# Performance work log

Measured on AMD Instinct MI355X. Metric: run time of the kernel, lower is better.

Reference implementation:

```python
import jax, jax.numpy as jnp
import numpy as np

EPS = 1e-8


def setup_inputs() -> dict:
    key = jax.random.key(0)
    ks = jax.random.split(key, 8)
    B, N, D = 8, 1024, 256
    x = jax.random.normal(ks[0], (B, N, D), dtype=jnp.float32)
    y = jax.random.normal(ks[1], (B, N, D), dtype=jnp.float32)
    coords = jax.random.normal(ks[2], (N, N, 6), dtype=jnp.float32)
    # xavier-ish init for U, kaiming-ish for S1/S2
    U = jax.random.normal(ks[3], (D, D), dtype=jnp.float32) * (1.0 / np.sqrt(D))
    S1 = jax.random.normal(ks[4], (D, 1), dtype=jnp.float32)
    S2 = jax.random.normal(ks[5], (D, 1), dtype=jnp.float32)
    gating = jnp.asarray(1.0, dtype=jnp.float32)
    h_temp = jnp.asarray(0.1, dtype=jnp.float32)
    p_temp = jnp.asarray(1.0, dtype=jnp.float32)
    # trunc_normal_(a=0, b=1): std-normal truncated to [0, 1]
    pos_emb = jax.random.truncated_normal(ks[6], 0.0, 1.0, (N, 6, 1)).astype(jnp.float32)
    return {"x": x, "y": y, "coords": coords, "U": U, "S1": S1, "S2": S2,
            "gating": gating, "h_temp": h_temp, "p_temp": p_temp, "pos_emb": pos_emb}


def _spectral(x, U, S):
    # x @ U.T @ diag(|S|) @ U  ==  ((x @ U.T) * |S|) @ U
    s = jnp.abs(S[:, 0])
    return ((x @ U.T) * s) @ U


def reference(x, y, coords, U, S1, S2, gating, h_temp, p_temp, pos_emb):
    B, N, D = x.shape
    scale = D ** (-0.5)
    xs = jnp.stack([_spectral(x, U, S1), _spectral(x, U, S2)], axis=1)  # [B,2,N,D]
    # patch attention scores: [B,2,N,N]
    patch_score = jax.nn.softmax(jnp.einsum('bknd,bmd->bknm', xs, y) * scale, axis=-1)
    # positional scores, shared across batch and the 2 spectral branches: [N,N]
    pos_logits = -jnp.abs(p_temp) * jnp.einsum('nmc,ncq->nm', coords, pos_emb)
    pos_score = jax.nn.softmax(pos_logits, axis=-1)
    g = jax.nn.sigmoid(gating)
    attn = (1.0 - g) * patch_score + g * pos_score[None, None]  # [B,2,N,N]
    # entropy over key axis -> [B,N,2]
    entropy = jnp.sum(-attn * jnp.log(attn + EPS), axis=-1).transpose(0, 2, 1)
    hmap = 2.0 - 2.0 * jax.nn.sigmoid(h_temp * entropy)  # [B,N,2]
    fgbg = hmap[..., 0] >= hmap[..., 1]
    route = jax.lax.stop_gradient(
        jnp.stack([fgbg, ~fgbg], axis=-1).astype(hmap.dtype))  # [B,N,2]
    heat_map = jnp.sum(hmap * route, axis=-1, keepdims=True)  # [B,N,1]
    attn_sel = jnp.sum(attn * route.transpose(0, 2, 1)[..., None], axis=1)  # [B,N,N]
    out = attn_sel @ y  # [B,N,D]
    return (out, heat_map)
```

## Files before the change

### kernel.cpp

```cpp
#include <hip/hip_runtime.h>
#include <hip/hip_bf16.h>
#include <stdint.h>


#define NB 8
#define NN_ 1024
#define ND 256

typedef __bf16 bf16x8 __attribute__((ext_vector_type(8)));
typedef __bf16 bf16x4 __attribute__((ext_vector_type(4)));
typedef float f32x4 __attribute__((ext_vector_type(4)));

__device__ inline void gl_lds(const __bf16* g, __bf16* l) {
    auto gp = (const __attribute__((address_space(1))) uint32_t*)(uintptr_t)g;
    auto lp = (__attribute__((address_space(3))) uint32_t*)(uintptr_t)l;
    __builtin_amdgcn_global_load_lds(gp, lp, 16, 0, 0);
}

__device__ inline float wred_sum(float v) {
#pragma unroll
    for (int o = 32; o; o >>= 1) v += __shfl_xor(v, o, 64);
    return v;
}
__device__ inline float wred_max(float v) {
#pragma unroll
    for (int o = 32; o; o >>= 1) v = fmaxf(v, __shfl_xor(v, o, 64));
    return v;
}
__device__ inline float bred_sum(float v, float* red) {
    v = wred_sum(v);
    int w = threadIdx.x >> 6;
    __syncthreads();
    if ((threadIdx.x & 63) == 0) red[w] = v;
    __syncthreads();
    return red[0] + red[1] + red[2] + red[3];
}
__device__ inline float bred_max(float v, float* red) {
    v = wred_max(v);
    int w = threadIdx.x >> 6;
    __syncthreads();
    if ((threadIdx.x & 63) == 0) red[w] = v;
    __syncthreads();
    return fmaxf(fmaxf(red[0], red[1]), fmaxf(red[2], red[3]));
}

__global__ __launch_bounds__(256) void pos_kernel(
    const float* __restrict__ coords, const float* __restrict__ pos_emb,
    const float* __restrict__ p_temp, float* __restrict__ posS) {
    __shared__ float red[4];
    const int n = blockIdx.x;
    const int tid = threadIdx.x;
    const float pt = -fabsf(p_temp[0]);
    float pe[6];
#pragma unroll
    for (int c = 0; c < 6; ++c) pe[c] = pos_emb[n * 6 + c];
    const float* cr = coords + (long)n * NN_ * 6;
    float l[4];
#pragma unroll
    for (int j = 0; j < 4; ++j) {
        const int m = j * 256 + tid;
        const float2* cp = (const float2*)(cr + (long)m * 6);
        float2 c0 = cp[0], c1 = cp[1], c2 = cp[2];
        l[j] = pt * (c0.x * pe[0] + c0.y * pe[1] + c1.x * pe[2] +
                     c1.y * pe[3] + c2.x * pe[4] + c2.y * pe[5]);
    }
    float mx = fmaxf(fmaxf(l[0], l[1]), fmaxf(l[2], l[3]));
    mx = bred_max(mx, red);
    float e[4], s = 0.f;
#pragma unroll
    for (int j = 0; j < 4; ++j) { e[j] = expf(l[j] - mx); s += e[j]; }
    s = bred_sum(s, red);
    const float inv = 1.f / s;
#pragma unroll
    for (int j = 0; j < 4; ++j) posS[(long)n * NN_ + j * 256 + tid] = e[j] * inv;
}

__global__ __launch_bounds__(256) void conv_split(
    const float* __restrict__ src, __bf16* __restrict__ hi,
    __bf16* __restrict__ lo, int n4) {
    int i = blockIdx.x * 256 + threadIdx.x;
    const int stride = gridDim.x * 256;
    for (; i < n4; i += stride) {
        float4 v = ((const float4*)src)[i];
        bf16x4 h, l;
        h[0] = (__bf16)v.x; l[0] = (__bf16)(v.x - (float)h[0]);
        h[1] = (__bf16)v.y; l[1] = (__bf16)(v.y - (float)h[1]);
        h[2] = (__bf16)v.z; l[2] = (__bf16)(v.z - (float)h[2]);
        h[3] = (__bf16)v.w; l[3] = (__bf16)(v.w - (float)h[3]);
        ((bf16x4*)hi)[i] = h;
        ((bf16x4*)lo)[i] = l;
    }
}

__global__ __launch_bounds__(256) void build_M(
    const float* __restrict__ U, const float* __restrict__ S1,
    const float* __restrict__ S2, __bf16* __restrict__ Mh,
    __bf16* __restrict__ Ml) {
    const int n = blockIdx.x, j = threadIdx.x;
    float a1 = 0.f, a2 = 0.f;
    for (int c = 0; c < ND; ++c) {
        const float un = U[c * ND + n];
        const float uj = U[c * ND + j];
        a1 = fmaf(fabsf(S1[c]) * un, uj, a1);
        a2 = fmaf(fabsf(S2[c]) * un, uj, a2);
    }
    const __bf16 h1 = (__bf16)a1, h2 = (__bf16)a2;
    Mh[n * ND + j] = h1;            Ml[n * ND + j] = (__bf16)(a1 - (float)h1);
    Mh[65536 + n * ND + j] = h2;    Ml[65536 + n * ND + j] = (__bf16)(a2 - (float)h2);
}

__global__ __launch_bounds__(256) void prep_y(
    const float* __restrict__ y, __bf16* __restrict__ yt,
    __bf16* __restrict__ Yh, __bf16* __restrict__ Yl) {
    __shared__ __bf16 t[64][72];
    const int b = blockIdx.z;
    const int m0 = blockIdx.x * 64, d0 = blockIdx.y * 64;
    const int tid = threadIdx.x;
    const int c = tid & 15;
    const int r = tid >> 4;
#pragma unroll
    for (int p = 0; p < 4; ++p) {
        const int row = r + p * 16;
        const long gi = ((long)b * NN_ + m0 + row) * ND + d0 + c * 4;
        float4 v = *(const float4*)(y + gi);
        bf16x4 h, l;
        h[0] = (__bf16)v.x; l[0] = (__bf16)(v.x - (float)h[0]);
        h[1] = (__bf16)v.y; l[1] = (__bf16)(v.y - (float)h[1]);
        h[2] = (__bf16)v.z; l[2] = (__bf16)(v.z - (float)h[2]);
        h[3] = (__bf16)v.w; l[3] = (__bf16)(v.w - (float)h[3]);
        *(bf16x4*)(Yh + gi) = h;
        *(bf16x4*)(Yl + gi) = l;
        t[c * 4 + 0][row] = h[0]; t[c * 4 + 1][row] = h[1];
        t[c * 4 + 2][row] = h[2]; t[c * 4 + 3][row] = h[3];
    }
    __syncthreads();
#pragma unroll
    for (int p = 0; p < 4; ++p) {
        const int d = r + p * 16;
        bf16x4 o;
        o[0] = t[d][c * 4 + 0]; o[1] = t[d][c * 4 + 1];
        o[2] = t[d][c * 4 + 2]; o[3] = t[d][c * 4 + 3];
        *(bf16x4*)(yt + ((long)b * ND + d0 + d) * NN_ + m0 + c * 4) = o;
    }
}

template <int BN, bool SPLIT, int OUTM>
__global__ __launch_bounds__(256) void mgemm(
    const __bf16* __restrict__ Ah, const __bf16* __restrict__ Al,
    const __bf16* __restrict__ Bh, const __bf16* __restrict__ Bl,
    float* __restrict__ C, __bf16* __restrict__ Ch, __bf16* __restrict__ Cl,
    int M, int N, int K,
    long sA1, long sA2, int divA, long sB1, int divB, long sC, float alpha) {
    constexpr int BM = 128, BK = 32;
    constexpr int NBUF = SPLIT ? 2 : 1;
    constexpr int NF = BN / 32;
    __shared__ __bf16 As[NBUF * BM * BK];
    __shared__ __bf16 Bs[NBUF * BN * BK];

    const int z = blockIdx.z;
    const long aoff = (long)(z / divA) * sA1 + (long)(z % divA) * sA2;
    const long boff = (long)(z / divB) * sB1;
    Ah += aoff; if (SPLIT) Al += aoff;
    Bh += boff; if (SPLIT) Bl += boff;

    const int tid = threadIdx.x;
    const int bm = blockIdx.y * BM, bn = blockIdx.x * BN;
    const int wave = tid >> 6, lane = tid & 63;
    const int wm = wave >> 1, wn = wave & 1;
    const int quad = lane >> 4, l16 = lane & 15;

    f32x4 acc[4][NF];
#pragma unroll
    for (int i = 0; i < 4; ++i)
#pragma unroll
        for (int j = 0; j < NF; ++j) acc[i][j] = (f32x4){0.f, 0.f, 0.f, 0.f};

    const int srow = lane >> 2;
    const int slot = lane & 3;

    for (int k0 = 0; k0 < K; k0 += BK) {
        __syncthreads();
#pragma unroll
        for (int i = 0; i < 2; ++i) {
            const int r0 = wave * 32 + i * 16;
            const int row = r0 + srow;
            const int chunk = slot ^ ((row >> 1) & 3);
            const long g = (long)(bm + row) * K + k0 + chunk * 8;
            gl_lds(Ah + g, &As[r0 * 32]);
            if (SPLIT) gl_lds(Al + g, &As[BM * BK + r0 * 32]);
        }
        if (BN == 128) {
#pragma unroll
            for (int i = 0; i < 2; ++i) {
                const int r0 = wave * 32 + i * 16;
                const int row = r0 + srow;
                const int chunk = slot ^ ((row >> 1) & 3);
                const long g = (long)(bn + row) * K + k0 + chunk * 8;
                gl_lds(Bh + g, &Bs[r0 * 32]);
                if (SPLIT) gl_lds(Bl + g, &Bs[BN * BK + r0 * 32]);
            }
        } else {
            const int r0 = wave * 16;
            const int row = r0 + srow;
            const int chunk = slot ^ ((row >> 1) & 3);
            const long g = (long)(bn + row) * K + k0 + chunk * 8;
            gl_lds(Bh + g, &Bs[r0 * 32]);
            if (SPLIT) gl_lds(Bl + g, &Bs[BN * BK + r0 * 32]);
        }
        __syncthreads();

        bf16x8 a_h[4], a_l[4], b_h[NF], b_l[NF];
#pragma unroll
        for (int mi = 0; mi < 4; ++mi) {
            const int row = wm * 64 + mi * 16 + l16;
            const int off = row * 32 + ((quad ^ ((row >> 1) & 3)) * 8);
            a_h[mi] = *(const bf16x8*)&As[off];
            if (SPLIT) a_l[mi] = *(const bf16x8*)&As[BM * BK + off];
        }
#pragma unroll
        for (int ni = 0; ni < NF; ++ni) {
            const int row = wn * (BN / 2) + ni * 16 + l16;
            const int off = row * 32 + ((quad ^ ((row >> 1) & 3)) * 8);
            b_h[ni] = *(const bf16x8*)&Bs[off];
            if (SPLIT) b_l[ni] = *(const bf16x8*)&Bs[BN * BK + off];
        }
#pragma unroll
        for (int mi = 0; mi < 4; ++mi)
#pragma unroll
            for (int ni = 0; ni < NF; ++ni) {
                acc[mi][ni] = __builtin_amdgcn_mfma_f32_16x16x32_bf16(
                    a_h[mi], b_h[ni], acc[mi][ni], 0, 0, 0);
                if (SPLIT) {
                    acc[mi][ni] = __builtin_amdgcn_mfma_f32_16x16x32_bf16(
                        a_h[mi], b_l[ni], acc[mi][ni], 0, 0, 0);
                    acc[mi][ni] = __builtin_amdgcn_mfma_f32_16x16x32_bf16(
                        a_l[mi], b_h[ni], acc[mi][ni], 0, 0, 0);
                }
            }
    }

    C += (long)z * sC; Ch += (long)z * sC; Cl += (long)z * sC;
#pragma unroll
    for (int mi = 0; mi < 4; ++mi) {
        const int row0 = bm + wm * 64 + mi * 16 + quad * 4;
#pragma unroll
        for (int ni = 0; ni < NF; ++ni) {
            const int col = bn + wn * (BN / 2) + ni * 16 + l16;
#pragma unroll
            for (int r = 0; r < 4; ++r) {
                const float v = acc[mi][ni][r] * alpha;
                const long idx = (long)(row0 + r) * N + col;
                if (OUTM == 0) {
                    C[idx] = v;
                } else {
                    const __bf16 h = (__bf16)v;
                    Ch[idx] = h;
                    Cl[idx] = (__bf16)(v - (float)h);
                }
            }
        }
    }
}

__global__ __launch_bounds__(256, 1) void mega_kernel(
    const __bf16* __restrict__ XSh, const __bf16* __restrict__ XSl,
    const __bf16* __restrict__ Yh, const __bf16* __restrict__ Yl,
    const __bf16* __restrict__ yt, const float* __restrict__ pos,
    const float* __restrict__ gating, const float* __restrict__ h_temp,
    float* __restrict__ heat, float* __restrict__ out) {
    extern __shared__ char smem[];
    __bf16* Pl  = (__bf16*)smem;
    float* red0 = (float*)(smem + 66048);
    float* red1 = red0 + 256;
    float* red2 = red1 + 256;

    const int b  = blockIdx.x & 7;
    const int n0 = (blockIdx.x >> 3) * 32;
    const int tid = threadIdx.x;
    const int wave = tid >> 6, lane = tid & 63;
    const int quad = lane >> 4, l16 = lane & 15;
    const int wcol = wave * 256;

    const __bf16* Ahp = XSh + ((long)b * NN_ + n0) * ND;
    const __bf16* Alp = XSl + ((long)b * NN_ + n0) * ND;
    const __bf16* Bhp = Yh + ((long)b * NN_ + wcol) * ND;
    const __bf16* Blp = Yl + ((long)b * NN_ + wcol) * ND;

    f32x4 acc[2][2][16];
#pragma unroll
    for (int br = 0; br < 2; ++br)
#pragma unroll
        for (int mi = 0; mi < 2; ++mi)
#pragma unroll
            for (int ni = 0; ni < 16; ++ni)
                acc[br][mi][ni] = (f32x4){0.f, 0.f, 0.f, 0.f};

    for (int k0 = 0; k0 < ND; k0 += 32) {
        bf16x8 ah[2][2], al[2][2];
#pragma unroll
        for (int br = 0; br < 2; ++br)
#pragma unroll
            for (int mi = 0; mi < 2; ++mi) {
                const long o = (long)br * (NB * NN_ * ND) +
                               (long)(mi * 16 + l16) * ND + k0 + quad * 8;
                ah[br][mi] = *(const bf16x8*)(Ahp + o);
                al[br][mi] = *(const bf16x8*)(Alp + o);
            }
#pragma unroll
        for (int ni = 0; ni < 16; ++ni) {
            const long o = (long)(ni * 16 + l16) * ND + k0 + quad * 8;
            bf16x8 bh = *(const bf16x8*)(Bhp + o);
            bf16x8 bl = *(const bf16x8*)(Blp + o);
#pragma unroll
            for (int br = 0; br < 2; ++br)
#pragma unroll
                for (int mi = 0; mi < 2; ++mi) {
                    acc[br][mi][ni] = __builtin_amdgcn_mfma_f32_16x16x32_bf16(
                        ah[br][mi], bh, acc[br][mi][ni], 0, 0, 0);
                    acc[br][mi][ni] = __builtin_amdgcn_mfma_f32_16x16x32_bf16(
                        ah[br][mi], bl, acc[br][mi][ni], 0, 0, 0);
                    acc[br][mi][ni] = __builtin_amdgcn_mfma_f32_16x16x32_bf16(
                        al[br][mi], bh, acc[br][mi][ni], 0, 0, 0);
                }
        }
    }

#pragma unroll
    for (int br = 0; br < 2; ++br)
#pragma unroll
        for (int mi = 0; mi < 2; ++mi)
#pragma unroll
            for (int ni = 0; ni < 16; ++ni)
#pragma unroll
                for (int rr = 0; rr < 4; ++rr)
                    acc[br][mi][ni][rr] *= 0.0625f;

    float mx[2][2][4];
#pragma unroll
    for (int br = 0; br < 2; ++br)
#pragma unroll
        for (int mi = 0; mi < 2; ++mi)
#pragma unroll
            for (int rr = 0; rr < 4; ++rr) {
                float m = -3.4e38f;
#pragma unroll
                for (int ni = 0; ni < 16; ++ni) m = fmaxf(m, acc[br][mi][ni][rr]);
                mx[br][mi][rr] = m;
            }
#pragma unroll
    for (int o = 1; o < 16; o <<= 1)
#pragma unroll
        for (int br = 0; br < 2; ++br)
#pragma unroll
            for (int mi = 0; mi < 2; ++mi)
#pragma unroll
                for (int rr = 0; rr < 4; ++rr)
                    mx[br][mi][rr] = fmaxf(mx[br][mi][rr],
                                           __shfl_xor(mx[br][mi][rr], o, 64));
    if (l16 == 0)
#pragma unroll
        for (int br = 0; br < 2; ++br)
#pragma unroll
            for (int mi = 0; mi < 2; ++mi)
#pragma unroll
                for (int rr = 0; rr < 4; ++rr)
                    red0[(wave * 2 + br) * 32 + mi * 16 + quad * 4 + rr] = mx[br][mi][rr];
    __syncthreads();
#pragma unroll
    for (int br = 0; br < 2; ++br)
#pragma unroll
        for (int mi = 0; mi < 2; ++mi)
#pragma unroll
            for (int rr = 0; rr < 4; ++rr) {
                const int ri = mi * 16 + quad * 4 + rr;
                float m = red0[(0 * 2 + br) * 32 + ri];
                m = fmaxf(m, red0[(1 * 2 + br) * 32 + ri]);
                m = fmaxf(m, red0[(2 * 2 + br) * 32 + ri]);
                m = fmaxf(m, red0[(3 * 2 + br) * 32 + ri]);
                mx[br][mi][rr] = m;
            }

    float sm[2][2][4];
#pragma unroll
    for (int br = 0; br < 2; ++br)
#pragma unroll
        for (int mi = 0; mi < 2; ++mi)
#pragma unroll
            for (int rr = 0; rr < 4; ++rr) {
                float s = 0.f;
#pragma unroll
                for (int ni = 0; ni < 16; ++ni) {
                    const float e = __expf(acc[br][mi][ni][rr] - mx[br][mi][rr]);
                    acc[br][mi][ni][rr] = e;
                    s += e;
                }
                sm[br][mi][rr] = s;
            }
#pragma unroll
    for (int o = 1; o < 16; o <<= 1)
#pragma unroll
        for (int br = 0; br < 2; ++br)
#pragma unroll
            for (int mi = 0; mi < 2; ++mi)
#pragma unroll
                for (int rr = 0; rr < 4; ++rr)
                    sm[br][mi][rr] += __shfl_xor(sm[br][mi][rr], o, 64);
    if (l16 == 0)
#pragma unroll
        for (int br = 0; br < 2; ++br)
#pragma unroll
            for (int mi = 0; mi < 2; ++mi)
#pragma unroll
                for (int rr = 0; rr < 4; ++rr)
                    red1[(wave * 2 + br) * 32 + mi * 16 + quad * 4 + rr] = sm[br][mi][rr];
    __syncthreads();
    float inv[2][2][4];
#pragma unroll
    for (int br = 0; br < 2; ++br)
#pragma unroll
        for (int mi = 0; mi < 2; ++mi)
#pragma unroll
            for (int rr = 0; rr < 4; ++rr) {
                const int ri = mi * 16 + quad * 4 + rr;
                const float s = red1[(0 * 2 + br) * 32 + ri] + red1[(1 * 2 + br) * 32 + ri] +
                                red1[(2 * 2 + br) * 32 + ri] + red1[(3 * 2 + br) * 32 + ri];
                inv[br][mi][rr] = 1.f / s;
            }

    const float g = 1.f / (1.f + __expf(-gating[0]));
    const float cg = 1.f - g;
    float ent[2][2][4];
#pragma unroll
    for (int br = 0; br < 2; ++br)
#pragma unroll
        for (int mi = 0; mi < 2; ++mi)
#pragma unroll
            for (int rr = 0; rr < 4; ++rr) ent[br][mi][rr] = 0.f;
#pragma unroll
    for (int mi = 0; mi < 2; ++mi)
#pragma unroll
        for (int ni = 0; ni < 16; ++ni)
#pragma unroll
            for (int rr = 0; rr < 4; ++rr) {
                const int ri = mi * 16 + quad * 4 + rr;
                const float pv = pos[(long)(n0 + ri) * NN_ + wcol + ni * 16 + l16];
#pragma unroll
                for (int br = 0; br < 2; ++br) {
                    const float a = cg * acc[br][mi][ni][rr] * inv[br][mi][rr] + g * pv;
                    acc[br][mi][ni][rr] = a;
                    ent[br][mi][rr] -= a * __logf(a + 1e-8f);
                }
            }
#pragma unroll
    for (int o = 1; o < 16; o <<= 1)
#pragma unroll
        for (int br = 0; br < 2; ++br)
#pragma unroll
            for (int mi = 0; mi < 2; ++mi)
#pragma unroll
                for (int rr = 0; rr < 4; ++rr)
                    ent[br][mi][rr] += __shfl_xor(ent[br][mi][rr], o, 64);
    if (l16 == 0)
#pragma unroll
        for (int br = 0; br < 2; ++br)
#pragma unroll
            for (int mi = 0; mi < 2; ++mi)
#pragma unroll
                for (int rr = 0; rr < 4; ++rr)
                    red2[(wave * 2 + br) * 32 + mi * 16 + quad * 4 + rr] = ent[br][mi][rr];
    __syncthreads();

    const float ht = h_temp[0];
    float fsel[2][4];
#pragma unroll
    for (int mi = 0; mi < 2; ++mi)
#pragma unroll
        for (int rr = 0; rr < 4; ++rr) {
            const int ri = mi * 16 + quad * 4 + rr;
            const float e0 = red2[0 * 32 + ri] + red2[2 * 32 + ri] +
                             red2[4 * 32 + ri] + red2[6 * 32 + ri];
            const float e1 = red2[1 * 32 + ri] + red2[3 * 32 + ri] +
                             red2[5 * 32 + ri] + red2[7 * 32 + ri];
            const float hm0 = 2.f - 2.f / (1.f + __expf(-ht * e0));
            const float hm1 = 2.f - 2.f / (1.f + __expf(-ht * e1));
            const bool fg = (hm0 >= hm1);
            fsel[mi][rr] = fg ? 1.f : 0.f;
            if (wave == 0 && l16 == 0)
                heat[(long)b * NN_ + n0 + ri] = fg ? hm0 : hm1;
        }
#pragma unroll
    for (int mi = 0; mi < 2; ++mi)
#pragma unroll
        for (int ni = 0; ni < 16; ++ni)
#pragma unroll
            for (int rr = 0; rr < 4; ++rr) {
                const int ri = mi * 16 + quad * 4 + rr;
                const float v = fsel[mi][rr] != 0.f ? acc[0][mi][ni][rr]
                                                    : acc[1][mi][ni][rr];
                Pl[ri * 1032 + wcol + ni * 16 + l16] = (__bf16)v;
            }
    __syncthreads();

    f32x4 oacc[2][4];
#pragma unroll
    for (int mi = 0; mi < 2; ++mi)
#pragma unroll
        for (int nd = 0; nd < 4; ++nd) oacc[mi][nd] = (f32x4){0.f, 0.f, 0.f, 0.f};
    const __bf16* Bo = yt + ((long)b * ND + wave * 64) * NN_;
    for (int k0 = 0; k0 < NN_; k0 += 32) {
        bf16x8 pa[2];
#pragma unroll
        for (int mi = 0; mi < 2; ++mi)
            pa[mi] = *(const bf16x8*)&Pl[(mi * 16 + l16) * 1032 + k0 + quad * 8];
#pragma unroll
        for (int nd = 0; nd < 4; ++nd) {
            bf16x8 bo = *(const bf16x8*)(Bo + (long)(nd * 16 + l16) * NN_ + k0 + quad * 8);
#pragma unroll
            for (int mi = 0; mi < 2; ++mi)
                oacc[mi][nd] = __builtin_amdgcn_mfma_f32_16x16x32_bf16(
                    pa[mi], bo, oacc[mi][nd], 0, 0, 0);
        }
    }
#pragma unroll
    for (int mi = 0; mi < 2; ++mi)
#pragma unroll
        for (int nd = 0; nd < 4; ++nd)
#pragma unroll
            for (int r = 0; r < 4; ++r)
                out[((long)b * NN_ + n0 + mi * 16 + quad * 4 + r) * ND +
                    wave * 64 + nd * 16 + l16] = oacc[mi][nd][r];
}

extern "C" void kernel_launch(void* const* d_in, const int* in_sizes, int n_in,
                              void* d_out, int out_size, void* d_ws, size_t ws_size,
                              hipStream_t stream) {
    const float* x      = (const float*)d_in[0];
    const float* y      = (const float*)d_in[1];
    const float* coords = (const float*)d_in[2];
    const float* U      = (const float*)d_in[3];
    const float* S1p    = (const float*)d_in[4];
    const float* S2p    = (const float*)d_in[5];
    const float* gating = (const float*)d_in[6];
    const float* h_temp = (const float*)d_in[7];
    const float* p_temp = (const float*)d_in[8];
    const float* pos_emb= (const float*)d_in[9];

    float* out  = (float*)d_out;
    float* heat = out + (long)NB * NN_ * ND;

    char* ws = (char*)d_ws;
    const long MB = 1 << 20;
    float*  pos = (float*)(ws);
    __bf16* Xh  = (__bf16*)(ws + 4 * MB);
    __bf16* Xl  = (__bf16*)(ws + 8 * MB);
    __bf16* XSh = (__bf16*)(ws + 12 * MB);
    __bf16* XSl = (__bf16*)(ws + 20 * MB);
    __bf16* yt  = (__bf16*)(ws + 28 * MB);
    __bf16* Yh  = (__bf16*)(ws + 32 * MB);
    __bf16* Yl  = (__bf16*)(ws + 36 * MB);
    __bf16* Mh  = (__bf16*)(ws + 40 * MB);
    __bf16* Ml  = Mh + 2 * 65536;

    const long ND2 = (long)NN_ * ND;
    const long BND = (long)NB * ND2;

    pos_kernel<<<dim3(NN_), 256, 0, stream>>>(coords, pos_emb, p_temp, pos);
    conv_split<<<dim3(2048), 256, 0, stream>>>(x, Xh, Xl, (int)(BND / 4));
    prep_y<<<dim3(16, 4, NB), 256, 0, stream>>>(y, yt, Yh, Yl);
    build_M<<<dim3(ND), ND, 0, stream>>>(U, S1p, S2p, Mh, Ml);

    mgemm<64, true, 1><<<dim3(4, 64, 2), 256, 0, stream>>>(
        Xh, Xl, Mh, Ml, nullptr, XSh, XSl, NB * NN_, ND, ND,
        0, 0, 1, 65536, 1, BND, 1.0f);

    hipFuncSetAttribute((const void*)mega_kernel,
                        hipFuncAttributeMaxDynamicSharedMemorySize, 69632);
    mega_kernel<<<dim3(256), 256, 69632, stream>>>(
        XSh, XSl, Yh, Yl, yt, pos, gating, h_temp, heat, out);

    (void)in_sizes; (void)n_in; (void)out_size; (void)ws_size;
}
```

Before: 229.6 us.

## Fuse prep kernels into one launch and halve mega_kernel row tile

Merges the four preprocessing kernels (pos softmax, x split, y split/transpose, M build) into a single launch that dispatches on block index, removing three kernel launches and their serialization gaps. The main fused attention kernel now processes 16 query rows per block instead of 32, doubling the grid to 512 blocks. It also switches to static shared memory and allows two blocks per CU, to improve occupancy and CU coverage. The trade-off is that each block re-reads the full Y tiles for only half as many rows, doubling B-operand traffic per output row.

```diff
diff --git a/kernel.cpp b/kernel.cpp
--- a/kernel.cpp
+++ b/kernel.cpp
@@ -27,120 +27,110 @@
     for (int o = 32; o; o >>= 1) v = fmaxf(v, __shfl_xor(v, o, 64));
     return v;
 }
-__device__ inline float bred_sum(float v, float* red) {
-    v = wred_sum(v);
-    int w = threadIdx.x >> 6;
-    __syncthreads();
-    if ((threadIdx.x & 63) == 0) red[w] = v;
-    __syncthreads();
-    return red[0] + red[1] + red[2] + red[3];
-}
-__device__ inline float bred_max(float v, float* red) {
-    v = wred_max(v);
-    int w = threadIdx.x >> 6;
-    __syncthreads();
-    if ((threadIdx.x & 63) == 0) red[w] = v;
-    __syncthreads();
-    return fmaxf(fmaxf(red[0], red[1]), fmaxf(red[2], red[3]));
-}
-
-__global__ __launch_bounds__(256) void pos_kernel(
+
+__global__ __launch_bounds__(256) void prep_kernel(
     const float* __restrict__ coords, const float* __restrict__ pos_emb,
-    const float* __restrict__ p_temp, float* __restrict__ posS) {
-    __shared__ float red[4];
-    const int n = blockIdx.x;
+    const float* __restrict__ p_temp, const float* __restrict__ x,
+    const float* __restrict__ y, const float* __restrict__ U,
+    const float* __restrict__ S1, const float* __restrict__ S2,
+    float* __restrict__ posS, __bf16* __restrict__ Xh, __bf16* __restrict__ Xl,
+    __bf16* __restrict__ yt, __bf16* __restrict__ Yh, __bf16* __restrict__ Yl,
+    __bf16* __restrict__ Mh, __bf16* __restrict__ Ml) {
+    __shared__ char sm[9216 + 64];
+    const int bid = blockIdx.x;
     const int tid = threadIdx.x;
-    const float pt = -fabsf(p_temp[0]);
-    float pe[6];
-#pragma unroll
-    for (int c = 0; c < 6; ++c) pe[c] = pos_emb[n * 6 + c];
-    const float* cr = coords + (long)n * NN_ * 6;
-    float l[4];
-#pragma unroll
-    for (int j = 0; j < 4; ++j) {
-        const int m = j * 256 + tid;
-        const float2* cp = (const float2*)(cr + (long)m * 6);
-        float2 c0 = cp[0], c1 = cp[1], c2 = cp[2];
-        l[j] = pt * (c0.x * pe[0] + c0.y * pe[1] + c1.x * pe[2] +
-                     c1.y * pe[3] + c2.x * pe[4] + c2.y * pe[5]);
-    }
-    float mx = fmaxf(fmaxf(l[0], l[1]), fmaxf(l[2], l[3]));
-    mx = bred_max(mx, red);
-    float e[4], s = 0.f;
-#pragma unroll
-    for (int j = 0; j < 4; ++j) { e[j] = expf(l[j] - mx); s += e[j]; }
-    s = bred_sum(s, red);
-    const float inv = 1.f / s;
-#pragma unroll
-    for (int j = 0; j < 4; ++j) posS[(long)n * NN_ + j * 256 + tid] = e[j] * inv;
-}
-
-__global__ __launch_bounds__(256) void conv_split(
-    const float* __restrict__ src, __bf16* __restrict__ hi,
-    __bf16* __restrict__ lo, int n4) {
-    int i = blockIdx.x * 256 + threadIdx.x;
-    const int stride = gridDim.x * 256;
-    for (; i < n4; i += stride) {
-        float4 v = ((const float4*)src)[i];
-        bf16x4 h, l;
-        h[0] = (__bf16)v.x; l[0] = (__bf16)(v.x - (float)h[0]);
-        h[1] = (__bf16)v.y; l[1] = (__bf16)(v.y - (float)h[1]);
-        h[2] = (__bf16)v.z; l[2] = (__bf16)(v.z - (float)h[2]);
-        h[3] = (__bf16)v.w; l[3] = (__bf16)(v.w - (float)h[3]);
-        ((bf16x4*)hi)[i] = h;
-        ((bf16x4*)lo)[i] = l;
-    }
-}
-
-__global__ __launch_bounds__(256) void build_M(
-    const float* __restrict__ U, const float* __restrict__ S1,
-    const float* __restrict__ S2, __bf16* __restrict__ Mh,
-    __bf16* __restrict__ Ml) {
-    const int n = blockIdx.x, j = threadIdx.x;
-    float a1 = 0.f, a2 = 0.f;
-    for (int c = 0; c < ND; ++c) {
-        const float un = U[c * ND + n];
-        const float uj = U[c * ND + j];
-        a1 = fmaf(fabsf(S1[c]) * un, uj, a1);
-        a2 = fmaf(fabsf(S2[c]) * un, uj, a2);
-    }
-    const __bf16 h1 = (__bf16)a1, h2 = (__bf16)a2;
-    Mh[n * ND + j] = h1;            Ml[n * ND + j] = (__bf16)(a1 - (float)h1);
-    Mh[65536 + n * ND + j] = h2;    Ml[65536 + n * ND + j] = (__bf16)(a2 - (float)h2);
-}
-
-__global__ __launch_bounds__(256) void prep_y(
-    const float* __restrict__ y, __bf16* __restrict__ yt,
-    __bf16* __restrict__ Yh, __bf16* __restrict__ Yl) {
-    __shared__ __bf16 t[64][72];
-    const int b = blockIdx.z;
-    const int m0 = blockIdx.x * 64, d0 = blockIdx.y * 64;
-    const int tid = threadIdx.x;
-    const int c = tid & 15;
-    const int r = tid >> 4;
-#pragma unroll
-    for (int p = 0; p < 4; ++p) {
-        const int row = r + p * 16;
-        const long gi = ((long)b * NN_ + m0 + row) * ND + d0 + c * 4;
-        float4 v = *(const float4*)(y + gi);
-        bf16x4 h, l;
-        h[0] = (__bf16)v.x; l[0] = (__bf16)(v.x - (float)h[0]);
-        h[1] = (__bf16)v.y; l[1] = (__bf16)(v.y - (float)h[1]);
-        h[2] = (__bf16)v.z; l[2] = (__bf16)(v.z - (float)h[2]);
-        h[3] = (__bf16)v.w; l[3] = (__bf16)(v.w - (float)h[3]);
-        *(bf16x4*)(Yh + gi) = h;
-        *(bf16x4*)(Yl + gi) = l;
-        t[c * 4 + 0][row] = h[0]; t[c * 4 + 1][row] = h[1];
-        t[c * 4 + 2][row] = h[2]; t[c * 4 + 3][row] = h[3];
-    }
-    __syncthreads();
-#pragma unroll
-    for (int p = 0; p < 4; ++p) {
-        const int d = r + p * 16;
-        bf16x4 o;
-        o[0] = t[d][c * 4 + 0]; o[1] = t[d][c * 4 + 1];
-        o[2] = t[d][c * 4 + 2]; o[3] = t[d][c * 4 + 3];
-        *(bf16x4*)(yt + ((long)b * ND + d0 + d) * NN_ + m0 + c * 4) = o;
+
+    if (bid < 1024) {
+        float* red = (float*)sm;
+        const int n = bid;
+        const float pt = -fabsf(p_temp[0]);
+        float pe[6];
+#pragma unroll
+        for (int c = 0; c < 6; ++c) pe[c] = pos_emb[n * 6 + c];
+        const float* cr = coords + (long)n * NN_ * 6;
+        float l[4];
+#pragma unroll
+        for (int j = 0; j < 4; ++j) {
+            const int m = j * 256 + tid;
+            const float2* cp = (const float2*)(cr + (long)m * 6);
+            float2 c0 = cp[0], c1 = cp[1], c2 = cp[2];
+            l[j] = pt * (c0.x * pe[0] + c0.y * pe[1] + c1.x * pe[2] +
+                         c1.y * pe[3] + c2.x * pe[4] + c2.y * pe[5]);
+        }
+        float mx = fmaxf(fmaxf(l[0], l[1]), fmaxf(l[2], l[3]));
+        mx = wred_max(mx);
+        __syncthreads();
+        if ((tid & 63) == 0) red[tid >> 6] = mx;
+        __syncthreads();
+        mx = fmaxf(fmaxf(red[0], red[1]), fmaxf(red[2], red[3]));
+        float e[4], s = 0.f;
+#pragma unroll
+        for (int j = 0; j < 4; ++j) { e[j] = __expf(l[j] - mx); s += e[j]; }
+        s = wred_sum(s);
+        __syncthreads();
+        if ((tid & 63) == 0) red[4 + (tid >> 6)] = s;
+        __syncthreads();
+        s = red[4] + red[5] + red[6] + red[7];
+        const float inv = 1.f / s;
+#pragma unroll
+        for (int j = 0; j < 4; ++j)
+            posS[(long)n * NN_ + j * 256 + tid] = e[j] * inv;
+    } else if (bid < 1536) {
+        const int n4 = NB * NN_ * ND / 4;
+        int i = (bid - 1024) * 256 + tid;
+        for (; i < n4; i += 512 * 256) {
+            float4 v = ((const float4*)x)[i];
+            bf16x4 h, l;
+            h[0] = (__bf16)v.x; l[0] = (__bf16)(v.x - (float)h[0]);
+            h[1] = (__bf16)v.y; l[1] = (__bf16)(v.y - (float)h[1]);
+            h[2] = (__bf16)v.z; l[2] = (__bf16)(v.z - (float)h[2]);
+            h[3] = (__bf16)v.w; l[3] = (__bf16)(v.w - (float)h[3]);
+            ((bf16x4*)Xh)[i] = h;
+            ((bf16x4*)Xl)[i] = l;
+        }
+    } else if (bid < 2048) {
+        __bf16 (*t)[72] = (__bf16(*)[72])sm;
+        const int rem = bid - 1536;
+        const int b = rem >> 6;
+        const int m0 = (rem & 15) * 64, d0 = ((rem >> 4) & 3) * 64;
+        const int c = tid & 15;
+        const int r = tid >> 4;
+#pragma unroll
+        for (int p = 0; p < 4; ++p) {
+            const int row = r + p * 16;
+            const long gi = ((long)b * NN_ + m0 + row) * ND + d0 + c * 4;
+            float4 v = *(const float4*)(y + gi);
+            bf16x4 h, l;
+            h[0] = (__bf16)v.x; l[0] = (__bf16)(v.x - (float)h[0]);
+            h[1] = (__bf16)v.y; l[1] = (__bf16)(v.y - (float)h[1]);
+            h[2] = (__bf16)v.z; l[2] = (__bf16)(v.z - (float)h[2]);
+            h[3] = (__bf16)v.w; l[3] = (__bf16)(v.w - (float)h[3]);
+            *(bf16x4*)(Yh + gi) = h;
+            *(bf16x4*)(Yl + gi) = l;
+            t[c * 4 + 0][row] = h[0]; t[c * 4 + 1][row] = h[1];
+            t[c * 4 + 2][row] = h[2]; t[c * 4 + 3][row] = h[3];
+        }
+        __syncthreads();
+#pragma unroll
+        for (int p = 0; p < 4; ++p) {
+            const int d = r + p * 16;
+            bf16x4 o;
+            o[0] = t[d][c * 4 + 0]; o[1] = t[d][c * 4 + 1];
+            o[2] = t[d][c * 4 + 2]; o[3] = t[d][c * 4 + 3];
+            *(bf16x4*)(yt + ((long)b * ND + d0 + d) * NN_ + m0 + c * 4) = o;
+        }
+    } else {
+        const int n = bid - 2048, j = tid;
+        float a1 = 0.f, a2 = 0.f;
+        for (int c = 0; c < ND; ++c) {
+            const float un = U[c * ND + n];
+            const float uj = U[c * ND + j];
+            a1 = fmaf(fabsf(S1[c]) * un, uj, a1);
+            a2 = fmaf(fabsf(S2[c]) * un, uj, a2);
+        }
+        const __bf16 h1 = (__bf16)a1, h2 = (__bf16)a2;
+        Mh[n * ND + j] = h1;           Ml[n * ND + j] = (__bf16)(a1 - (float)h1);
+        Mh[65536 + n * ND + j] = h2;   Ml[65536 + n * ND + j] = (__bf16)(a2 - (float)h2);
     }
 }
 
@@ -262,273 +252,214 @@
     }
 }
 
-__global__ __launch_bounds__(256, 1) void mega_kernel(
+__global__ __launch_bounds__(256, 2) void mega_kernel(
     const __bf16* __restrict__ XSh, const __bf16* __restrict__ XSl,
     const __bf16* __restrict__ Yh, const __bf16* __restrict__ Yl,
     const __bf16* __restrict__ yt, const float* __restrict__ pos,
     const float* __restrict__ gating, const float* __restrict__ h_temp,
     float* __restrict__ heat, float* __restrict__ out) {
-    extern __shared__ char smem[];
-    __bf16* Pl  = (__bf16*)smem;
-    float* red0 = (float*)(smem + 66048);
-    float* red1 = red0 + 256;
-    float* red2 = red1 + 256;
+    __shared__ __bf16 Pl[16 * 1032];
+    __shared__ float red0[128], red1[128], red2[128];
 
     const int b  = blockIdx.x & 7;
-    const int n0 = (blockIdx.x >> 3) * 32;
+    const int n0 = (blockIdx.x >> 3) * 16;
     const int tid = threadIdx.x;
     const int wave = tid >> 6, lane = tid & 63;
     const int quad = lane >> 4, l16 = lane & 15;
     const int wcol = wave * 256;
+    const long BNDe = (long)NB * NN_ * ND;
 
     const __bf16* Ahp = XSh + ((long)b * NN_ + n0) * ND;
     const __bf16* Alp = XSl + ((long)b * NN_ + n0) * ND;
     const __bf16* Bhp = Yh + ((long)b * NN_ + wcol) * ND;
     const __bf16* Blp = Yl + ((long)b * NN_ + wcol) * ND;
 
-    f32x4 acc[2][2][16];
+    f32x4 acc[2][16];
 #pragma unroll
     for (int br = 0; br < 2; ++br)
 #pragma unroll
-        for (int mi = 0; mi < 2; ++mi)
-#pragma unroll
-            for (int ni = 0; ni < 16; ++ni)
-                acc[br][mi][ni] = (f32x4){0.f, 0.f, 0.f, 0.f};
+        for (int ni = 0; ni < 16; ++ni) acc[br][ni] = (f32x4){0.f, 0.f, 0.f, 0.f};
 
     for (int k0 = 0; k0 < ND; k0 += 32) {
-        bf16x8 ah[2][2], al[2][2];
-#pragma unroll
-        for (int br = 0; br < 2; ++br)
-#pragma unroll
-            for (int mi = 0; mi < 2; ++mi) {
-                const long o = (long)br * (NB * NN_ * ND) +
-                               (long)(mi * 16 + l16) * ND + k0 + quad * 8;
-                ah[br][mi] = *(const bf16x8*)(Ahp + o);
-                al[br][mi] = *(const bf16x8*)(Alp + o);
-            }
+        bf16x8 ah[2], al[2];
+#pragma unroll
+        for (int br = 0; br < 2; ++br) {
+            const long o = (long)br * BNDe + (long)l16 * ND + k0 + quad * 8;
+            ah[br] = *(const bf16x8*)(Ahp + o);
+            al[br] = *(const bf16x8*)(Alp + o);
+        }
 #pragma unroll
         for (int ni = 0; ni < 16; ++ni) {
             const long o = (long)(ni * 16 + l16) * ND + k0 + quad * 8;
             bf16x8 bh = *(const bf16x8*)(Bhp + o);
             bf16x8 bl = *(const bf16x8*)(Blp + o);
 #pragma unroll
-            for (int br = 0; br < 2; ++br)
-#pragma unroll
-                for (int mi = 0; mi < 2; ++mi) {
-                    acc[br][mi][ni] = __builtin_amdgcn_mfma_f32_16x16x32_bf16(
-                        ah[br][mi], bh, acc[br][mi][ni], 0, 0, 0);
-                    acc[br][mi][ni] = __builtin_amdgcn_mfma_f32_16x16x32_bf16(
-                        ah[br][mi], bl, acc[br][mi][ni], 0, 0, 0);
-                    acc[br][mi][ni] = __builtin_amdgcn_mfma_f32_16x16x32_bf16(
-                        al[br][mi], bh, acc[br][mi][ni], 0, 0, 0);
-                }
+            for (int br = 0; br < 2; ++br) {
+                acc[br][ni] = __builtin_amdgcn_mfma_f32_16x16x32_bf16(
+                    ah[br], bh, acc[br][ni], 0, 0, 0);
+                acc[br][ni] = __builtin_amdgcn_mfma_f32_16x16x32_bf16(
+                    ah[br], bl, acc[br][ni], 0, 0, 0);
+                acc[br][ni] = __builtin_amdgcn_mfma_f32_16x16x32_bf16(
+                    al[br], bh, acc[br][ni], 0, 0, 0);
+            }
         }
     }
 
+    float mx[2][4];
 #pragma unroll
     for (int br = 0; br < 2; ++br)
 #pragma unroll
-        for (int mi = 0; mi < 2; ++mi)
-#pragma unroll
-            for (int ni = 0; ni < 16; ++ni)
-#pragma unroll
-                for (int rr = 0; rr < 4; ++rr)
-                    acc[br][mi][ni][rr] *= 0.0625f;
-
-    float mx[2][2][4];
+        for (int rr = 0; rr < 4; ++rr) {
+            float m = -3.4e38f;
+#pragma unroll
+            for (int ni = 0; ni < 16; ++ni) {
+                acc[br][ni][rr] *= 0.0625f;
+                m = fmaxf(m, acc[br][ni][rr]);
+            }
+            mx[br][rr] = m;
+        }
+#pragma unroll
+    for (int o = 1; o < 16; o <<= 1)
+#pragma unroll
+        for (int br = 0; br < 2; ++br)
+#pragma unroll
+            for (int rr = 0; rr < 4; ++rr)
+                mx[br][rr] = fmaxf(mx[br][rr], __shfl_xor(mx[br][rr], o, 64));
+    if (l16 == 0)
+#pragma unroll
+        for (int br = 0; br < 2; ++br)
+#pragma unroll
+            for (int rr = 0; rr < 4; ++rr)
+                red0[(wave * 2 + br) * 16 + quad * 4 + rr] = mx[br][rr];
+    __syncthreads();
 #pragma unroll
     for (int br = 0; br < 2; ++br)
 #pragma unroll
-        for (int mi = 0; mi < 2; ++mi)
-#pragma unroll
-            for (int rr = 0; rr < 4; ++rr) {
-                float m = -3.4e38f;
-#pragma unroll
-                for (int ni = 0; ni < 16; ++ni) m = fmaxf(m, acc[br][mi][ni][rr]);
-                mx[br][mi][rr] = m;
-            }
+        for (int rr = 0; rr < 4; ++rr) {
+            const int ri = quad * 4 + rr;
+            float m = red0[(0 + br) * 16 + ri];
+            m = fmaxf(m, red0[(2 + br) * 16 + ri]);
+            m = fmaxf(m, red0[(4 + br) * 16 + ri]);
+            m = fmaxf(m, red0[(6 + br) * 16 + ri]);
+            mx[br][rr] = m;
+        }
+
+    float sm[2][4];
+#pragma unroll
+    for (int br = 0; br < 2; ++br)
+#pragma unroll
+        for (int rr = 0; rr < 4; ++rr) {
+            float s = 0.f;
+#pragma unroll
+            for (int ni = 0; ni < 16; ++ni) {
+                const float e = __expf(acc[br][ni][rr] - mx[br][rr]);
+                acc[br][ni][rr] = e;
+                s += e;
+            }
+            sm[br][rr] = s;
+        }
 #pragma unroll
     for (int o = 1; o < 16; o <<= 1)
 #pragma unroll
         for (int br = 0; br < 2; ++br)
 #pragma unroll
-            for (int mi = 0; mi < 2; ++mi)
-#pragma unroll
-                for (int rr = 0; rr < 4; ++rr)
-                    mx[br][mi][rr] = fmaxf(mx[br][mi][rr],
-                                           __shfl_xor(mx[br][mi][rr], o, 64));
+            for (int rr = 0; rr < 4; ++rr)
+                sm[br][rr] += __shfl_xor(sm[br][rr], o, 64);
     if (l16 == 0)
 #pragma unroll
         for (int br = 0; br < 2; ++br)
 #pragma unroll
-            for (int mi = 0; mi < 2; ++mi)
-#pragma unroll
-                for (int rr = 0; rr < 4; ++rr)
-                    red0[(wave * 2 + br) * 32 + mi * 16 + quad * 4 + rr] = mx[br][mi][rr];
+            for (int rr = 0; rr < 4; ++rr)
+                red1[(wave * 2 + br) * 16 + quad * 4 + rr] = sm[br][rr];
     __syncthreads();
+    float inv[2][4];
 #pragma unroll
     for (int br = 0; br < 2; ++br)
 #pragma unroll
-        for (int mi = 0; mi < 2; ++mi)
-#pragma unroll
-            for (int rr = 0; rr < 4; ++rr) {
-                const int ri = mi * 16 + quad * 4 + rr;
-                float m = red0[(0 * 2 + br) * 32 + ri];
-                m = fmaxf(m, red0[(1 * 2 + br) * 32 + ri]);
-                m = fmaxf(m, red0[(2 * 2 + br) * 32 + ri]);
-                m = fmaxf(m, red0[(3 * 2 + br) * 32 + ri]);
-                mx[br][mi][rr] = m;
-            }
-
-    float sm[2][2][4];
-#pragma unroll
-    for (int br = 0; br < 2; ++br)
-#pragma unroll
-        for (int mi = 0; mi < 2; ++mi)
-#pragma unroll
-            for (int rr = 0; rr < 4; ++rr) {
-                float s = 0.f;
-#pragma unroll
-                for (int ni = 0; ni < 16; ++ni) {
-                    const float e = __expf(acc[br][mi][ni][rr] - mx[br][mi][rr]);
-                    acc[br][mi][ni][rr] = e;
-                    s += e;
-                }
-                sm[br][mi][rr] = s;
-            }
-#pragma unroll
-    for (int o = 1; o < 16; o <<= 1)
-#pragma unroll
-        for (int br = 0; br < 2; ++br)
-#pragma unroll
-            for (int mi = 0; mi < 2; ++mi)
-#pragma unroll
-                for (int rr = 0; rr < 4; ++rr)
-                    sm[br][mi][rr] += __shfl_xor(sm[br][mi][rr], o, 64);
-    if (l16 == 0)
-#pragma unroll
-        for (int br = 0; br < 2; ++br)
-#pragma unroll
-            for (int mi = 0; mi < 2; ++mi)
-#pragma unroll
-                for (int rr = 0; rr < 4; ++rr)
-                    red1[(wave * 2 + br) * 32 + mi * 16 + quad * 4 + rr] = sm[br][mi][rr];
-    __syncthreads();
-    float inv[2][2][4];
-#pragma unroll
-    for (int br = 0; br < 2; ++br)
-#pragma unroll
-        for (int mi = 0; mi < 2; ++mi)
-#pragma unroll
-            for (int rr = 0; rr < 4; ++rr) {
-                const int ri = mi * 16 + quad * 4 + rr;
-                const float s = red1[(0 * 2 + br) * 32 + ri] + red1[(1 * 2 + br) * 32 + ri] +
-                                red1[(2 * 2 + br) * 32 + ri] + red1[(3 * 2 + br) * 32 + ri];
-                inv[br][mi][rr] = 1.f / s;
-            }
+        for (int rr = 0; rr < 4; ++rr) {
+            const int ri = quad * 4 + rr;
+            const float s = red1[(0 + br) * 16 + ri] + red1[(2 + br) * 16 + ri] +
+                            red1[(4 + br) * 16 + ri] + red1[(6 + br) * 16 + ri];
+            inv[br][rr] = 1.f / s;
+        }
 
     const float g = 1.f / (1.f + __expf(-gating[0]));
     const float cg = 1.f - g;
-    float ent[2][2][4];
+    float ent[2][4];
 #pragma unroll
     for (int br = 0; br < 2; ++br)
 #pragma unroll
-        for (int mi = 0; mi < 2; ++mi)
-#pragma unroll
-            for (int rr = 0; rr < 4; ++rr) ent[br][mi][rr] = 0.f;
-#pragma unroll
-    for (int mi = 0; mi < 2; ++mi)
-#pragma unroll
-        for (int ni = 0; ni < 16; ++ni)
-#pragma unroll
-            for (int rr = 0; rr < 4; ++rr) {
-                const int ri = mi * 16 + quad * 4 + rr;
-                const float pv = pos[(long)(n0 + ri) * NN_ + wcol + ni * 16 + l16];
-#pragma unroll
-                for (int br = 0; br < 2; ++br) {
-                    const float a = cg * acc[br][mi][ni][rr] * inv[br][mi][rr] + g * pv;
-                    acc[br][mi][ni][rr] = a;
-                    ent[br][mi][rr] -= a * __logf(a + 1e-8f);
-                }
-            }
+        for (int rr = 0; rr < 4; ++rr) ent[br][rr] = 0.f;
+#pragma unroll
+    for (int ni = 0; ni < 16; ++ni)
+#pragma unroll
+        for (int rr = 0; rr < 4; ++rr) {
+            const int ri = quad * 4 + rr;
+            const float pv = pos[(long)(n0 + ri) * NN_ + wcol + ni * 16 + l16];
+#pragma unroll
+            for (int br = 0; br < 2; ++br) {
+                const float a = cg * acc[br][ni][rr] * inv[br][rr] + g * pv;
+                acc[br][ni][rr] = a;
+                ent[br][rr] -= a * __logf(a + 1e-8f);
+            }
+        }
 #pragma unroll
     for (int o = 1; o < 16; o <<= 1)
 #pragma unroll
         for (int br = 0; br < 2; ++br)
 #pragma unroll
-            for (int mi = 0; mi < 2; ++mi)
-#pragma unroll
-                for (int rr = 0; rr < 4; ++rr)
-                    ent[br][mi][rr] += __shfl_xor(ent[br][mi][rr], o, 64);
+            for (int rr = 0; rr < 4; ++rr)
+                ent[br][rr] += __shfl_xor(ent[br][rr], o, 64);
     if (l16 == 0)
 #pragma unroll
         for (int br = 0; br < 2; ++br)
 #pragma unroll
-            for (int mi = 0; mi < 2; ++mi)
-#pragma unroll
-                for (int rr = 0; rr < 4; ++rr)
-                    red2[(wave * 2 + br) * 32 + mi * 16 + quad * 4 + rr] = ent[br][mi][rr];
+            for (int rr = 0; rr < 4; ++rr)
+                red2[(wave * 2 + br) * 16 + quad * 4 + rr] = ent[br][rr];
     __syncthreads();
 
     const float ht = h_temp[0];
-    float fsel[2][4];
-#pragma unroll
-    for (int mi = 0; mi < 2; ++mi)
+    float fsel[4];
+#pragma unroll
+    for (int rr = 0; rr < 4; ++rr) {
+        const int ri = quad * 4 + rr;
+        const float e0 = red2[0 + ri] + red2[32 + ri] + red2[64 + ri] + red2[96 + ri];
+        const float e1 = red2[16 + ri] + red2[48 + ri] + red2[80 + ri] + red2[112 + ri];
+        const float hm0 = 2.f - 2.f / (1.f + __expf(-ht * e0));
+        const float hm1 = 2.f - 2.f / (1.f + __expf(-ht * e1));
+        const bool fg = (hm0 >= hm1);
+        fsel[rr] = fg ? 1.f : 0.f;
+        if (wave == 0 && l16 == 0)
+            heat[(long)b * NN_ + n0 + ri] = fg ? hm0 : hm1;
+    }
+#pragma unroll
+    for (int ni = 0; ni < 16; ++ni)
 #pragma unroll
         for (int rr = 0; rr < 4; ++rr) {
-            const int ri = mi * 16 + quad * 4 + rr;
-            const float e0 = red2[0 * 32 + ri] + red2[2 * 32 + ri] +
-                             red2[4 * 32 + ri] + red2[6 * 32 + ri];
-            const float e1 = red2[1 * 32 + ri] + red2[3 * 32 + ri] +
-                             red2[5 * 32 + ri] + red2[7 * 32 + ri];
-            const float hm0 = 2.f - 2.f / (1.f + __expf(-ht * e0));
-            const float hm1 = 2.f - 2.f / (1.f + __expf(-ht * e1));
-            const bool fg = (hm0 >= hm1);
-            fsel[mi][rr] = fg ? 1.f : 0.f;
-            if (wave == 0 && l16 == 0)
-                heat[(long)b * NN_ + n0 + ri] = fg ? hm0 : hm1;
-        }
-#pragma unroll
-    for (int mi = 0; mi < 2; ++mi)
-#pragma unroll
-        for (int ni = 0; ni < 16; ++ni)
-#pragma unroll
-            for (int rr = 0; rr < 4; ++rr) {
-                const int ri = mi * 16 + quad * 4 + rr;
-                const float v = fsel[mi][rr] != 0.f ? acc[0][mi][ni][rr]
-                                                    : acc[1][mi][ni][rr];
-                Pl[ri * 1032 + wcol + ni * 16 + l16] = (__bf16)v;
-            }
+            const int ri = quad * 4 + rr;
+            const float v = fsel[rr] != 0.f ? acc[0][ni][rr] : acc[1][ni][rr];
+            Pl[ri * 1032 + wcol + ni * 16 + l16] = (__bf16)v;
+        }
     __syncthreads();
 
-    f32x4 oacc[2][4];
-#pragma unroll
-    for (int mi = 0; mi < 2; ++mi)
-#pragma unroll
-        for (int nd = 0; nd < 4; ++nd) oacc[mi][nd] = (f32x4){0.f, 0.f, 0.f, 0.f};
+    f32x4 oacc[4];
+#pragma unroll
+    for (int nd = 0; nd < 4; ++nd) oacc[nd] = (f32x4){0.f, 0.f, 0.f, 0.f};
     const __bf16* Bo = yt + ((long)b * ND + wave * 64) * NN_;
     for (int k0 = 0; k0 < NN_; k0 += 32) {
-        bf16x8 pa[2];
-#pragma unroll
-        for (int mi = 0; mi < 2; ++mi)
-            pa[mi] = *(const bf16x8*)&Pl[(mi * 16 + l16) * 1032 + k0 + quad * 8];
+        bf16x8 pa = *(const bf16x8*)&Pl[l16 * 1032 + k0 + quad * 8];
 #pragma unroll
         for (int nd = 0; nd < 4; ++nd) {
             bf16x8 bo = *(const bf16x8*)(Bo + (long)(nd * 16 + l16) * NN_ + k0 + quad * 8);
-#pragma unroll
-            for (int mi = 0; mi < 2; ++mi)
-                oacc[mi][nd] = __builtin_amdgcn_mfma_f32_16x16x32_bf16(
-                    pa[mi], bo, oacc[mi][nd], 0, 0, 0);
+            oacc[nd] = __builtin_amdgcn_mfma_f32_16x16x32_bf16(pa, bo, oacc[nd], 0, 0, 0);
         }
     }
 #pragma unroll
-    for (int mi = 0; mi < 2; ++mi)
-#pragma unroll
-        for (int nd = 0; nd < 4; ++nd)
-#pragma unroll
-            for (int r = 0; r < 4; ++r)
-                out[((long)b * NN_ + n0 + mi * 16 + quad * 4 + r) * ND +
-                    wave * 64 + nd * 16 + l16] = oacc[mi][nd][r];
+    for (int nd = 0; nd < 4; ++nd)
+#pragma unroll
+        for (int r = 0; r < 4; ++r)
+            out[((long)b * NN_ + n0 + quad * 4 + r) * ND +
+                wave * 64 + nd * 16 + l16] = oacc[nd][r];
 }
 
 extern "C" void kernel_launch(void* const* d_in, const int* in_sizes, int n_in,
@@ -561,21 +492,17 @@
     __bf16* Mh  = (__bf16*)(ws + 40 * MB);
     __bf16* Ml  = Mh + 2 * 65536;
 
-    const long ND2 = (long)NN_ * ND;
-    const long BND = (long)NB * ND2;
-
-    pos_kernel<<<dim3(NN_), 256, 0, stream>>>(coords, pos_emb, p_temp, pos);
-    conv_split<<<dim3(2048), 256, 0, stream>>>(x, Xh, Xl, (int)(BND / 4));
-    prep_y<<<dim3(16, 4, NB), 256, 0, stream>>>(y, yt, Yh, Yl);
-    build_M<<<dim3(ND), ND, 0, stream>>>(U, S1p, S2p, Mh, Ml);
+    const long BND = (long)NB * NN_ * ND;
+
+    prep_kernel<<<dim3(2304), 256, 0, stream>>>(
+        coords, pos_emb, p_temp, x, y, U, S1p, S2p,
+        pos, Xh, Xl, yt, Yh, Yl, Mh, Ml);
 
     mgemm<64, true, 1><<<dim3(4, 64, 2), 256, 0, stream>>>(
         Xh, Xl, Mh, Ml, nullptr, XSh, XSl, NB * NN_, ND, ND,
         0, 0, 1, 65536, 1, BND, 1.0f);
 
-    hipFuncSetAttribute((const void*)mega_kernel,
-                        hipFuncAttributeMaxDynamicSharedMemorySize, 69632);
-    mega_kernel<<<dim3(256), 256, 69632, stream>>>(
+    mega_kernel<<<dim3(512), 256, 0, stream>>>(
         XSh, XSl, Yh, Yl, yt, pos, gating, h_temp, heat, out);
 
     (void)in_sizes; (void)n_in; (void)out_size; (void)ws_size;
```

New measurement: 236.5 us. 3.0% more time.
